# Kernel optimization log

Hardware: AMD Instinct MI355X
Metric: run time of the kernel (lower is better)

Reference implementation:

```python
import jax, jax.numpy as jnp
import numpy as np

BIT_W = 8   # config.bit_wt
BIT_A = 8   # config.bit_act (activations sliced 2 bits at a time)
STRIDE = (1, 1)
PAD = 1


def _conv(a, w):
    # NCHW input, OIHW weight, stride 1, symmetric padding 1 (matches wrapped Conv2d)
    return jax.lax.conv_general_dilated(
        a, w, window_strides=STRIDE, padding=[(PAD, PAD), (PAD, PAD)],
        dimension_numbers=("NCHW", "OIHW", "NCHW"))


def setup_inputs() -> dict:
    key = jax.random.key(0)
    k1, k2, k3 = jax.random.split(key, 3)
    x = jax.random.normal(k1, (64, 64, 56, 56), dtype=jnp.float32)
    weight = jax.random.normal(k2, (64, 64, 3, 3), dtype=jnp.float32)
    bias = jax.random.normal(k3, (64,), dtype=jnp.float32)
    scale_a = jnp.full((1,), 20.0, dtype=jnp.float32)      # conv_q.scale
    scale_w = jnp.full((1,), 20.0, dtype=jnp.float32)      # wrapped_module.weight_scale
    zero_point = jnp.full((1,), -128.0, dtype=jnp.float32)  # conv_q.zero_point
    return {"x": x, "weight": weight, "bias": bias,
            "scale_a": scale_a, "scale_w": scale_w, "zero_point": zero_point}


def reference(x, weight, bias, scale_a, scale_w, zero_point):
    sa = scale_a[0]
    sw = scale_w[0]
    zp = zero_point[0]
    # activation quantization: round(x*scale_a - zero_point), clamp to [0, 2^bit_act - 1]
    q_in = jnp.clip(jnp.round(x * sa - zp), 0.0, 2.0 ** BIT_A - 1.0)
    # weight quantization: round(w * scale_w), interpreted in two's complement
    q_w = jnp.round(weight * sw)
    w_off = q_w + 2.0 ** BIT_W  # (w + (1 << bit_weight)) before bit masking

    acc = jnp.zeros((), dtype=jnp.float32)
    for ba in range(BIT_A // 2):
        # 2-bit activation slice: (a >> 2*ba) & 3
        a_sl = jnp.mod(jnp.floor(q_in / (4.0 ** ba)), 4.0)
        for bw in range(BIT_W):
            # weight bit bw: ((w + 2^B) >> bw) & 1
            w_bit = jnp.mod(jnp.floor(w_off / (2.0 ** bw)), 2.0)
            r = _conv(a_sl, w_bit)
            sgn = -1.0 if bw == BIT_W - 1 else 1.0  # MSB = sign bit (two's complement)
            acc = acc + sgn * (2.0 ** (2 * ba + bw)) * r

    # zero-point correction: conv(ones * zp, q_w) added back (no-op when zp == 0)
    acc = acc + zp * _conv(jnp.ones_like(q_in), q_w)

    out = acc / (sw * sa) + bias[None, :, None, None]
    return out
```

## Files before the change

### kernel.cpp

```cpp
#include <hip/hip_runtime.h>


typedef int v4i  __attribute__((ext_vector_type(4)));
typedef int v16i __attribute__((ext_vector_type(16)));

#define QA_ROW   3712
#define QA_IMG   215296
#define QA_BYTES 13778944

__global__ __launch_bounds__(64) void prep_wq(const float* __restrict__ wt,
                                              const float* __restrict__ sw_p,
                                              signed char* __restrict__ w8,
                                              int* __restrict__ Qtc,
                                              int* __restrict__ Qraw) {
  const int o = blockIdx.x;
  const int i = threadIdx.x;
  const float sw = sw_p[0];
  const float* wp = wt + (size_t)(o * 64 + i) * 9;
  int q[9];
#pragma unroll
  for (int k = 0; k < 9; ++k) q[k] = (int)rintf(wp[k] * sw);
#pragma unroll
  for (int k = 0; k < 9; ++k)
    w8[(o * 9 + k) * 64 + i] = (signed char)(q[k] & 255);
#pragma unroll
  for (int k = 0; k < 9; ++k) {
    int stc = (int)(signed char)(q[k] & 255);
    int srw = q[k];
#pragma unroll
    for (int off = 32; off; off >>= 1) {
      stc += __shfl_xor(stc, off);
      srw += __shfl_xor(srw, off);
    }
    if (i == 0) { Qtc[o * 9 + k] = stc; Qraw[o * 9 + k] = srw; }
  }
}

__global__ __launch_bounds__(256) void quant_a(const float* __restrict__ x,
                                               const float* __restrict__ sa_p,
                                               const float* __restrict__ zp_p,
                                               signed char* __restrict__ qa) {
  __shared__ int ldsbuf[1904];
  signed char* lds = (signed char*)ldsbuf;
  const int bx = blockIdx.x;
  const int n = blockIdx.y;
  const int t = threadIdx.x;
  const float sa = sa_p[0], zp = zp_p[0];
  const float* xim = x + (size_t)n * 200704;
  const int h0 = bx * 2;

#pragma unroll
  for (int it = 0; it < 7; ++it) {
    const int idx = t + 256 * it;
    const int r = idx >= 896;
    const int rem = idx - 896 * r;
    const int c = (rem * 2341) >> 15;
    const int w4 = rem - c * 14;
    const float4 v = *(const float4*)(xim + (size_t)c * 3136 + (h0 + r) * 56 + w4 * 4);
    signed char* dst = lds + r * 3808 + w4 * 272 + c;
    const float vv[4] = {v.x, v.y, v.z, v.w};
#pragma unroll
    for (int e = 0; e < 4; ++e) {
      float tq;
      {
#pragma clang fp contract(off)
        tq = vv[e] * sa - zp;
      }
      float qf = rintf(tq);
      qf = fminf(fmaxf(qf, 0.0f), 255.0f);
      dst[e * 68] = (signed char)((int)qf - 128);
    }
  }
  __syncthreads();

  signed char* const qim = qa + (size_t)n * QA_IMG;
#pragma unroll
  for (int it = 0; it < 2; ++it) {
    const int idx = t + 256 * it;
    if (idx < 448) {
      const int r = idx >= 224;
      const int u = idx - 224 * r;
      const int w = u >> 2, q2 = u & 3;
      const unsigned* s = (const unsigned*)(lds + r * 3808 + w * 68 + q2 * 16);
      const uint4 vv = make_uint4(s[0], s[1], s[2], s[3]);
      *((uint4*)(qim + (size_t)(h0 + r + 1) * QA_ROW + (w + 1) * 64 + q2 * 16)) = vv;
    } else if (idx < 464) {
      const int p = idx - 448;
      const int r = p >> 3;
      const int side = (p >> 2) & 1;
      const int j = p & 3;
      *((uint4*)(qim + (size_t)(h0 + r + 1) * QA_ROW + side * 57 * 64 + j * 16)) =
          make_uint4(0, 0, 0, 0);
    }
  }
  if (bx == 0 && t < 232)
    ((uint4*)qim)[t] = make_uint4(0, 0, 0, 0);
  if (bx == 27 && t < 232)
    ((uint4*)(qim + (size_t)57 * QA_ROW))[t] = make_uint4(0, 0, 0, 0);
}

__global__ __launch_bounds__(256) void conv_mfma(
    const signed char* __restrict__ qa, const signed char* __restrict__ w8,
    const int* __restrict__ Qtc, const int* __restrict__ Qraw,
    const float* __restrict__ bias, const float* __restrict__ sa_p,
    const float* __restrict__ sw_p, const float* __restrict__ zp_p,
    float* __restrict__ out) {
  const int tid = threadIdx.x;
  const int lane = tid & 63;
  const int wv = tid >> 6;
  const int og = wv & 1;
  const int nsub = wv >> 1;
  const int n = blockIdx.y * 2 + nsub;
  const int p0 = blockIdx.x * 64;
  const int ln = lane & 31;
  const int lhi = lane >> 5;
  const int o = og * 32 + ln;

  const signed char* wb = w8 + (size_t)o * 576 + lhi * 16;
  v4i B[9][2];
#pragma unroll
  for (int tp = 0; tp < 9; ++tp)
#pragma unroll
    for (int kk = 0; kk < 2; ++kk)
      B[tp][kk] = *(const v4i*)(wb + tp * 64 + kk * 32);

  const float sa = sa_p[0], sw = sw_p[0], zp = zp_p[0];
  float ct[9];
#pragma unroll
  for (int k = 0; k < 9; ++k)
    ct[k] = 128.0f * (float)Qtc[o * 9 + k] + zp * (float)Qraw[o * 9 + k];
  const float Full = ct[0] + ct[1] + ct[2] + ct[3] + ct[4] + ct[5] + ct[6] + ct[7] + ct[8];
  const float Rtop = ct[0] + ct[1] + ct[2];
  const float Rbot = ct[6] + ct[7] + ct[8];
  const float Clft = ct[0] + ct[3] + ct[6];
  const float Crgt = ct[2] + ct[5] + ct[8];
  const float rden = 1.0f / (sw * sa);
  const float bo = bias[o];

  const signed char* qim = qa + (size_t)n * QA_IMG + lhi * 16;
  float* const obase = out + (size_t)(n * 64 + o) * 3136;

#pragma unroll
  for (int st = 0; st < 2; ++st) {
    const int pxa = p0 + st * 32 + ln;
    const int hp = (pxa * 9363) >> 19;
    const int wp = pxa - hp * 56;
    const signed char* abase = qim + (hp * 58 + wp) * 64;
    v16i acc = {0, 0, 0, 0, 0, 0, 0, 0, 0, 0, 0, 0, 0, 0, 0, 0};
#pragma unroll
    for (int kh = 0; kh < 3; ++kh) {
#pragma unroll
      for (int kw = 0; kw < 3; ++kw) {
        const signed char* ap = abase + kh * QA_ROW + kw * 64;
        const v4i a0 = *(const v4i*)(ap);
        const v4i a1 = *(const v4i*)(ap + 32);
        acc = __builtin_amdgcn_mfma_i32_32x32x32_i8(a0, B[kh * 3 + kw][0], acc, 0, 0, 0);
        acc = __builtin_amdgcn_mfma_i32_32x32x32_i8(a1, B[kh * 3 + kw][1], acc, 0, 0, 0);
      }
    }
#pragma unroll
    for (int q2 = 0; q2 < 4; ++q2) {
      const int pxb = p0 + st * 32 + 8 * q2 + 4 * lhi;
      float tmp[4];
#pragma unroll
      for (int e = 0; e < 4; ++e) {
        const int p = pxb + e;
        const int h = (p * 9363) >> 19;
        const int w = p - h * 56;
        const bool tb = (h == 0), bb = (h == 55), lb = (w == 0), rb = (w == 55);
        float corr = Full;
        corr -= tb ? Rtop : 0.0f;
        corr -= bb ? Rbot : 0.0f;
        corr -= lb ? Clft : 0.0f;
        corr -= rb ? Crgt : 0.0f;
        corr += (tb && lb) ? ct[0] : 0.0f;
        corr += (tb && rb) ? ct[2] : 0.0f;
        corr += (bb && lb) ? ct[6] : 0.0f;
        corr += (bb && rb) ? ct[8] : 0.0f;
        tmp[e] = ((float)acc[4 * q2 + e] + corr) * rden + bo;
      }
      float4 vv;
      vv.x = tmp[0]; vv.y = tmp[1]; vv.z = tmp[2]; vv.w = tmp[3];
      *(float4*)(obase + pxb) = vv;
    }
  }
}

extern "C" void kernel_launch(void* const* d_in, const int* in_sizes, int n_in,
                              void* d_out, int out_size, void* d_ws, size_t ws_size,
                              hipStream_t stream) {
  const float* x    = (const float*)d_in[0];
  const float* wt   = (const float*)d_in[1];
  const float* bias = (const float*)d_in[2];
  const float* sa   = (const float*)d_in[3];
  const float* sw   = (const float*)d_in[4];
  const float* zp   = (const float*)d_in[5];
  float* out = (float*)d_out;

  char* ws = (char*)d_ws;
  signed char* qa = (signed char*)ws;
  signed char* w8 = (signed char*)(ws + QA_BYTES);
  int* Qtc  = (int*)(ws + QA_BYTES + 36864);
  int* Qraw = (int*)(ws + QA_BYTES + 36864 + 2304);

  prep_wq<<<64, 64, 0, stream>>>(wt, sw, w8, Qtc, Qraw);
  quant_a<<<dim3(28, 64), 256, 0, stream>>>(x, sa, zp, qa);
  conv_mfma<<<dim3(49, 32), 256, 0, stream>>>(qa, w8, Qtc, Qraw, bias, sa, sw, zp, out);
}
```

Baseline: 140.6 us.

## Switch conv to 16x16x64 int8 MFMA tiles with one image per block

Replaces the 32x32x32 int8 MFMA tiling with 16x16x64 MFMAs: each wave now covers 16 output channels and loops over four 16-pixel tiles, so each 3x3 tap needs one MFMA instead of two. Each block handles a single image with four channel groups, doubling the grid, and the register footprint drops (one v4i accumulator, 9 B registers) while launch bounds request 4 blocks per CU for higher occupancy. An interior fast path skips the border zero-point correction math. The trade-off is that the activation tile is re-read by the four channel-group waves and each tile is processed serially with less unrolling.

```diff
diff --git a/kernel.cpp b/kernel.cpp
--- a/kernel.cpp
+++ b/kernel.cpp
@@ -1,8 +1,7 @@
 #include <hip/hip_runtime.h>
 
 
-typedef int v4i  __attribute__((ext_vector_type(4)));
-typedef int v16i __attribute__((ext_vector_type(16)));
+typedef int v4i __attribute__((ext_vector_type(4)));
 
 #define QA_ROW   3712
 #define QA_IMG   215296
@@ -99,7 +98,7 @@
     ((uint4*)(qim + (size_t)57 * QA_ROW))[t] = make_uint4(0, 0, 0, 0);
 }
 
-__global__ __launch_bounds__(256) void conv_mfma(
+__global__ __launch_bounds__(256, 4) void conv_mfma(
     const signed char* __restrict__ qa, const signed char* __restrict__ w8,
     const int* __restrict__ Qtc, const int* __restrict__ Qraw,
     const float* __restrict__ bias, const float* __restrict__ sa_p,
@@ -107,22 +106,17 @@
     float* __restrict__ out) {
   const int tid = threadIdx.x;
   const int lane = tid & 63;
-  const int wv = tid >> 6;
-  const int og = wv & 1;
-  const int nsub = wv >> 1;
-  const int n = blockIdx.y * 2 + nsub;
+  const int og = tid >> 6;
+  const int n = blockIdx.y;
   const int p0 = blockIdx.x * 64;
-  const int ln = lane & 31;
-  const int lhi = lane >> 5;
-  const int o = og * 32 + ln;
-
-  const signed char* wb = w8 + (size_t)o * 576 + lhi * 16;
-  v4i B[9][2];
-#pragma unroll
-  for (int tp = 0; tp < 9; ++tp)
-#pragma unroll
-    for (int kk = 0; kk < 2; ++kk)
-      B[tp][kk] = *(const v4i*)(wb + tp * 64 + kk * 32);
+  const int ln = lane & 15;
+  const int kg = lane >> 4;
+  const int o = og * 16 + ln;
+
+  const signed char* wbp = w8 + (size_t)o * 576 + kg * 16;
+  v4i B[9];
+#pragma unroll
+  for (int tp = 0; tp < 9; ++tp) B[tp] = *(const v4i*)(wbp + tp * 64);
 
   const float sa = sa_p[0], sw = sw_p[0], zp = zp_p[0];
   float ct[9];
@@ -134,34 +128,40 @@
   const float Rbot = ct[6] + ct[7] + ct[8];
   const float Clft = ct[0] + ct[3] + ct[6];
   const float Crgt = ct[2] + ct[5] + ct[8];
+  const float c0 = ct[0], c2 = ct[2], c6 = ct[6], c8 = ct[8];
   const float rden = 1.0f / (sw * sa);
   const float bo = bias[o];
 
-  const signed char* qim = qa + (size_t)n * QA_IMG + lhi * 16;
+  const signed char* qim = qa + (size_t)n * QA_IMG + kg * 16;
   float* const obase = out + (size_t)(n * 64 + o) * 3136;
 
-#pragma unroll
-  for (int st = 0; st < 2; ++st) {
-    const int pxa = p0 + st * 32 + ln;
+#pragma unroll 1
+  for (int t = 0; t < 4; ++t) {
+    const int pxa = p0 + t * 16 + ln;
     const int hp = (pxa * 9363) >> 19;
     const int wp = pxa - hp * 56;
     const signed char* abase = qim + (hp * 58 + wp) * 64;
-    v16i acc = {0, 0, 0, 0, 0, 0, 0, 0, 0, 0, 0, 0, 0, 0, 0, 0};
-#pragma unroll
-    for (int kh = 0; kh < 3; ++kh) {
-#pragma unroll
-      for (int kw = 0; kw < 3; ++kw) {
-        const signed char* ap = abase + kh * QA_ROW + kw * 64;
-        const v4i a0 = *(const v4i*)(ap);
-        const v4i a1 = *(const v4i*)(ap + 32);
-        acc = __builtin_amdgcn_mfma_i32_32x32x32_i8(a0, B[kh * 3 + kw][0], acc, 0, 0, 0);
-        acc = __builtin_amdgcn_mfma_i32_32x32x32_i8(a1, B[kh * 3 + kw][1], acc, 0, 0, 0);
-      }
-    }
-#pragma unroll
-    for (int q2 = 0; q2 < 4; ++q2) {
-      const int pxb = p0 + st * 32 + 8 * q2 + 4 * lhi;
-      float tmp[4];
+    v4i A[9];
+#pragma unroll
+    for (int kh = 0; kh < 3; ++kh)
+#pragma unroll
+      for (int kw = 0; kw < 3; ++kw)
+        A[kh * 3 + kw] = *(const v4i*)(abase + kh * QA_ROW + kw * 64);
+
+    v4i acc = {0, 0, 0, 0};
+#pragma unroll
+    for (int k = 0; k < 9; ++k)
+      acc = __builtin_amdgcn_mfma_i32_16x16x64_i8(A[k], B[k], acc, 0, 0, 0);
+
+    const int pxb = p0 + t * 16 + kg * 4;
+    const int hb = (pxb * 9363) >> 19;
+    const int wb2 = pxb - hb * 56;
+    float tmp[4];
+    if (hb >= 1 && hb <= 54 && wb2 >= 1 && wb2 <= 51) {
+#pragma unroll
+      for (int e = 0; e < 4; ++e)
+        tmp[e] = ((float)acc[e] + Full) * rden + bo;
+    } else {
 #pragma unroll
       for (int e = 0; e < 4; ++e) {
         const int p = pxb + e;
@@ -173,16 +173,16 @@
         corr -= bb ? Rbot : 0.0f;
         corr -= lb ? Clft : 0.0f;
         corr -= rb ? Crgt : 0.0f;
-        corr += (tb && lb) ? ct[0] : 0.0f;
-        corr += (tb && rb) ? ct[2] : 0.0f;
-        corr += (bb && lb) ? ct[6] : 0.0f;
-        corr += (bb && rb) ? ct[8] : 0.0f;
-        tmp[e] = ((float)acc[4 * q2 + e] + corr) * rden + bo;
+        corr += (tb && lb) ? c0 : 0.0f;
+        corr += (tb && rb) ? c2 : 0.0f;
+        corr += (bb && lb) ? c6 : 0.0f;
+        corr += (bb && rb) ? c8 : 0.0f;
+        tmp[e] = ((float)acc[e] + corr) * rden + bo;
       }
-      float4 vv;
-      vv.x = tmp[0]; vv.y = tmp[1]; vv.z = tmp[2]; vv.w = tmp[3];
-      *(float4*)(obase + pxb) = vv;
-    }
+    }
+    float4 vv;
+    vv.x = tmp[0]; vv.y = tmp[1]; vv.z = tmp[2]; vv.w = tmp[3];
+    *(float4*)(obase + pxb) = vv;
   }
 }
 
@@ -205,5 +205,5 @@
 
   prep_wq<<<64, 64, 0, stream>>>(wt, sw, w8, Qtc, Qraw);
   quant_a<<<dim3(28, 64), 256, 0, stream>>>(x, sa, zp, qa);
-  conv_mfma<<<dim3(49, 32), 256, 0, stream>>>(qa, w8, Qtc, Qraw, bias, sa, sw, zp, out);
-}
+  conv_mfma<<<dim3(49, 64), 256, 0, stream>>>(qa, w8, Qtc, Qraw, bias, sa, sw, zp, out);
+}
```

Result: slower. 145.8 us (+3.7%).
